# Optimization experiments

Measured on AMD Instinct MI355X. Metric: run time of the kernel, lower is better.

## Reference

```python
import jax, jax.numpy as jnp
import numpy as np

E, G, H = 500000, 256, 256
FRONTIER_BONUS = 0.5
LN_EPS = 1e-5


def setup_inputs() -> dict:
    key = jax.random.key(0)
    ks = jax.random.split(key, 10)
    s = 1.0 / np.sqrt(H)
    edge_tokens = jax.random.normal(ks[0], (E, H), dtype=jnp.float32)
    question_tokens = jax.random.normal(ks[1], (G, H), dtype=jnp.float32)
    edge_batch = jnp.sort(jax.random.randint(ks[2], (E,), 0, G))
    selected_mask = jax.random.randint(ks[3], (E,), 0, 2) == 1
    W_edge = (jax.random.normal(ks[4], (H, H)) * s).astype(jnp.float32)
    W_query = (jax.random.normal(ks[5], (H, H)) * s).astype(jnp.float32)
    att_vec = (jax.random.normal(ks[6], (H,)) * s).astype(jnp.float32)
    ln_g = jnp.ones((2 * H,), jnp.float32)
    ln_b = jnp.zeros((2 * H,), jnp.float32)
    W1 = (jax.random.normal(ks[7], (H, 2 * H)) * (1.0 / np.sqrt(2 * H))).astype(jnp.float32)
    b1 = jnp.zeros((H,), jnp.float32)
    W2 = (jax.random.normal(ks[8], (1, H)) * s).astype(jnp.float32)
    b2 = jnp.zeros((1,), jnp.float32)
    return dict(edge_tokens=edge_tokens, question_tokens=question_tokens,
                edge_batch=edge_batch, selected_mask=selected_mask,
                W_edge=W_edge, W_query=W_query, att_vec=att_vec,
                ln_g=ln_g, ln_b=ln_b, W1=W1, b1=b1, W2=W2, b2=b2)


def reference(edge_tokens, question_tokens, edge_batch, selected_mask,
              W_edge, W_query, att_vec, ln_g, ln_b, W1, b1, W2, b2):
    eps = jnp.finfo(jnp.float32).eps
    candidate_mask = ~selected_mask                      # [E]
    frontier_mask = candidate_mask                       # no current_tail path

    edge_h = edge_tokens @ W_edge.T                      # [E, H]
    q_h = question_tokens @ W_query.T                    # [G, H]

    att_inp = edge_h + q_h[edge_batch]                   # [E, H]
    att_raw = att_inp @ att_vec                          # [E]
    att_raw = jnp.where(att_raw > 0, att_raw, 0.2 * att_raw)  # LeakyReLU(0.2)
    att_raw = att_raw + FRONTIER_BONUS * frontier_mask.astype(jnp.float32)

    # segment softmax over candidate edges of each graph
    max_per_graph = jax.ops.segment_max(att_raw, edge_batch, num_segments=G)
    norm_logits = att_raw - max_per_graph[edge_batch]
    exp = jnp.exp(norm_logits) * candidate_mask.astype(jnp.float32)
    sum_per_graph = jax.ops.segment_sum(exp, edge_batch, num_segments=G)
    edge_probs = exp / jnp.maximum(sum_per_graph, eps)[edge_batch]
    # dropout in eval mode -> identity
    edge_logits = jnp.log(jnp.maximum(edge_probs, eps))  # [E]

    # mean pooling of edge_h per graph
    denom = jnp.maximum(jnp.bincount(edge_batch, length=G), 1).astype(jnp.float32)  # [G]
    pooled_edges = jax.ops.segment_sum(edge_h, edge_batch, num_segments=G) / denom[:, None]

    # stop head: LayerNorm(2H) -> Linear -> GELU -> Linear(1)
    stop_input = jnp.concatenate([pooled_edges, question_tokens], axis=-1)  # [G, 2H]
    mu = stop_input.mean(-1, keepdims=True)
    var = ((stop_input - mu) ** 2).mean(-1, keepdims=True)
    xn = (stop_input - mu) * jax.lax.rsqrt(var + LN_EPS) * ln_g + ln_b
    h1 = jax.nn.gelu(xn @ W1.T + b1, approximate=False)
    stop_logits = (h1 @ W2.T + b2).squeeze(-1)           # [G]

    return edge_logits, stop_logits, pooled_edges
```

## Files before the change

### kernel.cpp

```cpp
#include <hip/hip_runtime.h>
#include <math.h>

#define H   256
#define H2  512
#define FRONTIER_BONUS 0.5f
#define LN_EPS   1e-5f
#define F32_EPS  1.1920929e-07f

__device__ __forceinline__ float block_sum_256(float v, float* sbuf) {
    int tid = threadIdx.x;
    sbuf[tid] = v; __syncthreads();
    for (int s = 128; s > 0; s >>= 1) {
        if (tid < s) sbuf[tid] += sbuf[tid + s];
        __syncthreads();
    }
    float r = sbuf[0]; __syncthreads();
    return r;
}

__device__ __forceinline__ float block_max_256(float v, float* sbuf) {
    int tid = threadIdx.x;
    sbuf[tid] = v; __syncthreads();
    for (int s = 128; s > 0; s >>= 1) {
        if (tid < s) sbuf[tid] = fmaxf(sbuf[tid], sbuf[tid + s]);
        __syncthreads();
    }
    float r = sbuf[0]; __syncthreads();
    return r;
}

__device__ __forceinline__ float wave_sum(float p) {
    #pragma unroll
    for (int off = 1; off < 64; off <<= 1) p += __shfl_xor(p, off, 64);
    return p;
}

__global__ __launch_bounds__(H) void k_uw(const float* __restrict__ W_edge,
                                          const float* __restrict__ W_query,
                                          const float* __restrict__ att_vec,
                                          float* __restrict__ u,
                                          float* __restrict__ w) {
    const float* W = (blockIdx.x == 0) ? W_edge : W_query;
    float* dst     = (blockIdx.x == 0) ? u : w;
    int j = threadIdx.x;
    float acc = 0.f;
    #pragma unroll 8
    for (int i = 0; i < H; ++i) acc += att_vec[i] * W[i * H + j];
    dst[j] = acc;
}

__global__ __launch_bounds__(H) void k_qatt(const float* __restrict__ q,
                                            const float* __restrict__ w,
                                            float* __restrict__ qatt,
                                            float* __restrict__ pooled_sum) {
    __shared__ float sbuf[256];
    int g = blockIdx.x, tid = threadIdx.x;
    pooled_sum[(size_t)g * H + tid] = 0.f;
    float v = q[(size_t)g * H + tid] * w[tid];
    float s = block_sum_256(v, sbuf);
    if (tid == 0) qatt[g] = s;
}

__global__ __launch_bounds__(256) void k_main(const float* __restrict__ edge_tokens,
                                              const int*   __restrict__ edge_batch,
                                              const int*   __restrict__ selected,
                                              const float* __restrict__ u,
                                              const float* __restrict__ qatt,
                                              float* __restrict__ att_raw,
                                              float* __restrict__ pooled_sum,
                                              int E, int chunk) {
    int wave = (blockIdx.x * blockDim.x + threadIdx.x) >> 6;
    int lane = threadIdx.x & 63;
    int e0 = wave * chunk;
    if (e0 >= E) return;
    int e1 = e0 + chunk; if (e1 > E) e1 = E;

    const float4 u4 = ((const float4*)u)[lane];
    const float4* et = (const float4*)edge_tokens;
    float4 acc = make_float4(0.f, 0.f, 0.f, 0.f);
    int cur = edge_batch[e0];

    int e = e0;
    while (e < e1) {
        int n = e1 - e; if (n > 64) n = 64;
        int idx = e + ((lane < n) ? lane : (n - 1));
        int gb  = edge_batch[idx];
        int sel = selected[idx];
        int g0  = __shfl(gb, 0, 64);
        unsigned long long diff = __ballot(gb != g0);
        int run = n;
        if (diff) { int f = (int)__ffsll(diff) - 1; if (f < run) run = f; }

        if (g0 != cur) {
            float* dst = pooled_sum + (size_t)cur * H + lane * 4;
            atomicAdd(dst + 0, acc.x); atomicAdd(dst + 1, acc.y);
            atomicAdd(dst + 2, acc.z); atomicAdd(dst + 3, acc.w);
            acc = make_float4(0.f, 0.f, 0.f, 0.f);
            cur = g0;
        }
        float qa = qatt[g0];
        float my_att = 0.f;

        #pragma unroll 4
        for (int i = 0; i < run; ++i) {
            float4 t = et[(size_t)(e + i) * 64 + lane];
            acc.x += t.x; acc.y += t.y; acc.z += t.z; acc.w += t.w;
            float p = fmaf(t.x, u4.x, fmaf(t.y, u4.y, fmaf(t.z, u4.z, t.w * u4.w)));
            p = wave_sum(p);
            if (i == lane) my_att = p;
        }

        if (lane < run) {
            float a = my_att + qa;
            a = (a > 0.f) ? a : 0.2f * a;
            if (sel == 0) a += FRONTIER_BONUS;
            att_raw[e + lane] = a;
        }
        e += run;
    }
    float* dst = pooled_sum + (size_t)cur * H + lane * 4;
    atomicAdd(dst + 0, acc.x); atomicAdd(dst + 1, acc.y);
    atomicAdd(dst + 2, acc.z); atomicAdd(dst + 3, acc.w);
}

__global__ __launch_bounds__(256) void k_seg(const int*   __restrict__ edge_batch,
                                             const int*   __restrict__ selected,
                                             const float* __restrict__ att_raw,
                                             float* __restrict__ edge_logits,
                                             int*   __restrict__ gcount,
                                             int E) {
    __shared__ float sbuf[256];
    __shared__ int srange[2];
    int g = blockIdx.x, tid = threadIdx.x;
    if (tid == 0) {
        int lo = 0, hi = E;
        while (lo < hi) { int m = (lo + hi) >> 1; if (edge_batch[m] < g) lo = m + 1; else hi = m; }
        srange[0] = lo;
        hi = E;
        while (lo < hi) { int m = (lo + hi) >> 1; if (edge_batch[m] < g + 1) lo = m + 1; else hi = m; }
        srange[1] = lo;
    }
    __syncthreads();
    int s = srange[0], t = srange[1];

    float m = -INFINITY;
    for (int e = s + tid; e < t; e += 256) m = fmaxf(m, att_raw[e]);
    m = block_max_256(m, sbuf);

    float ss = 0.f;
    for (int e = s + tid; e < t; e += 256)
        if (selected[e] == 0) ss += expf(att_raw[e] - m);
    ss = block_sum_256(ss, sbuf);
    float denom = fmaxf(ss, F32_EPS);

    for (int e = s + tid; e < t; e += 256) {
        float ex = (selected[e] == 0) ? expf(att_raw[e] - m) : 0.f;
        float p  = ex / denom;
        edge_logits[e] = logf(fmaxf(p, F32_EPS));
    }
    if (tid == 0) gcount[g] = t - s;
}

__global__ __launch_bounds__(256) void k_pool(const float* __restrict__ pooled_sum,
                                              const int*   __restrict__ gcount,
                                              const float* __restrict__ q,
                                              const float* __restrict__ W_edge,
                                              const float* __restrict__ ln_g,
                                              const float* __restrict__ ln_b,
                                              const float* __restrict__ W1,
                                              const float* __restrict__ b1,
                                              const float* __restrict__ W2,
                                              const float* __restrict__ b2,
                                              float* __restrict__ pooled_out,
                                              float* __restrict__ stop_out) {
    __shared__ __align__(16) float sS[H];
    __shared__ __align__(16) float sP[H];
    __shared__ __align__(16) float sxn[H2];
    __shared__ __align__(16) float sgk[H];
    __shared__ float sbuf[256];
    int g = blockIdx.x, tid = threadIdx.x;
    int lane = tid & 63, wv = tid >> 6;

    sS[tid] = pooled_sum[(size_t)g * H + tid];
    __syncthreads();
    int   cnt = gcount[g];
    float inv = 1.f / (float)(cnt > 1 ? cnt : 1);

    float4 s4 = ((const float4*)sS)[lane];
    for (int r = 0; r < 64; ++r) {
        int i = wv * 64 + r;
        float4 w4 = ((const float4*)(W_edge + (size_t)i * H))[lane];
        float p = fmaf(w4.x, s4.x, fmaf(w4.y, s4.y, fmaf(w4.z, s4.z, w4.w * s4.w)));
        p = wave_sum(p);
        if (lane == 0) sP[i] = p * inv;
    }
    __syncthreads();
    float P = sP[tid];
    pooled_out[(size_t)g * H + tid] = P;

    float x1 = q[(size_t)g * H + tid];
    float mu  = block_sum_256(P + x1, sbuf) * (1.f / (float)H2);
    float d0 = P - mu, d1 = x1 - mu;
    float var = block_sum_256(d0 * d0 + d1 * d1, sbuf) * (1.f / (float)H2);
    float rstd = rsqrtf(var + LN_EPS);
    sxn[tid]     = d0 * rstd * ln_g[tid]     + ln_b[tid];
    sxn[tid + H] = d1 * rstd * ln_g[tid + H] + ln_b[tid + H];
    __syncthreads();

    float4 xa = ((const float4*)sxn)[lane];
    float4 xb = ((const float4*)sxn)[lane + 64];
    for (int r = 0; r < 64; ++r) {
        int k = wv * 64 + r;
        const float4* w1r = (const float4*)(W1 + (size_t)k * H2);
        float4 a0 = w1r[lane], a1 = w1r[lane + 64];
        float p = fmaf(a0.x, xa.x, fmaf(a0.y, xa.y, fmaf(a0.z, xa.z, a0.w * xa.w)))
                + fmaf(a1.x, xb.x, fmaf(a1.y, xb.y, fmaf(a1.z, xb.z, a1.w * xb.w)));
        p = wave_sum(p);
        if (lane == 0) {
            float a = p + b1[k];
            float ge = 0.5f * a * (1.f + erff(a * 0.70710678118654752f));
            sgk[k] = ge * W2[k];
        }
    }
    __syncthreads();
    float tot = block_sum_256(sgk[tid], sbuf);
    if (tid == 0) stop_out[g] = tot + b2[0];
}

extern "C" void kernel_launch(void* const* d_in, const int* in_sizes, int n_in,
                              void* d_out, int out_size, void* d_ws, size_t ws_size,
                              hipStream_t stream) {
    const float* edge_tokens     = (const float*)d_in[0];
    const float* question_tokens = (const float*)d_in[1];
    const int*   edge_batch      = (const int*)  d_in[2];
    const int*   selected        = (const int*)  d_in[3];
    const float* W_edge          = (const float*)d_in[4];
    const float* W_query         = (const float*)d_in[5];
    const float* att_vec         = (const float*)d_in[6];
    const float* ln_g            = (const float*)d_in[7];
    const float* ln_b            = (const float*)d_in[8];
    const float* W1              = (const float*)d_in[9];
    const float* b1              = (const float*)d_in[10];
    const float* W2              = (const float*)d_in[11];
    const float* b2              = (const float*)d_in[12];

    const int E = in_sizes[2];
    const int G = in_sizes[1] / H;

    float* out         = (float*)d_out;
    float* edge_logits = out;
    float* stop_out    = out + E;
    float* pooled_out  = out + E + G;

    float* ws         = (float*)d_ws;
    float* att_raw    = ws;
    float* pooled_sum = ws + E;
    float* u          = pooled_sum + (size_t)G * H;
    float* w          = u + H;
    float* qatt       = w + H;
    int*   gcount     = (int*)(qatt + G);

    k_uw  <<<2, H, 0, stream>>>(W_edge, W_query, att_vec, u, w);
    k_qatt<<<G, H, 0, stream>>>(question_tokens, w, qatt, pooled_sum);

    const int nblocks = 1024;
    const int waves   = nblocks * (256 / 64);
    const int chunk   = (E + waves - 1) / waves;
    k_main<<<nblocks, 256, 0, stream>>>(edge_tokens, edge_batch, selected,
                                        u, qatt, att_raw, pooled_sum, E, chunk);

    k_seg <<<G, 256, 0, stream>>>(edge_batch, selected, att_raw,
                                  edge_logits, gcount, E);
    k_pool<<<G, 256, 0, stream>>>(pooled_sum, gcount, question_tokens, W_edge,
                                  ln_g, ln_b, W1, b1, W2, b2,
                                  pooled_out, stop_out);
}
```

Before: 820.1 us.

## Fuse prologue and epilogue kernels, use nontemporal loads, double main grid

```diff
diff --git a/kernel.cpp b/kernel.cpp
--- a/kernel.cpp
+++ b/kernel.cpp
@@ -6,6 +6,8 @@
 #define FRONTIER_BONUS 0.5f
 #define LN_EPS   1e-5f
 #define F32_EPS  1.1920929e-07f
+
+typedef float v4f __attribute__((ext_vector_type(4)));
 
 __device__ __forceinline__ float block_sum_256(float v, float* sbuf) {
     int tid = threadIdx.x;
@@ -35,28 +37,28 @@
     return p;
 }
 
-__global__ __launch_bounds__(H) void k_uw(const float* __restrict__ W_edge,
-                                          const float* __restrict__ W_query,
-                                          const float* __restrict__ att_vec,
-                                          float* __restrict__ u,
-                                          float* __restrict__ w) {
-    const float* W = (blockIdx.x == 0) ? W_edge : W_query;
-    float* dst     = (blockIdx.x == 0) ? u : w;
-    int j = threadIdx.x;
-    float acc = 0.f;
-    #pragma unroll 8
-    for (int i = 0; i < H; ++i) acc += att_vec[i] * W[i * H + j];
-    dst[j] = acc;
-}
-
-__global__ __launch_bounds__(H) void k_qatt(const float* __restrict__ q,
-                                            const float* __restrict__ w,
-                                            float* __restrict__ qatt,
-                                            float* __restrict__ pooled_sum) {
+__global__ __launch_bounds__(256) void k_pro(const float* __restrict__ W_edge,
+                                             const float* __restrict__ W_query,
+                                             const float* __restrict__ att_vec,
+                                             const float* __restrict__ q,
+                                             float* __restrict__ u,
+                                             float* __restrict__ qatt,
+                                             float* __restrict__ pooled_sum,
+                                             int G) {
     __shared__ float sbuf[256];
     int g = blockIdx.x, tid = threadIdx.x;
+    if (g == G) {
+        float acc = 0.f;
+        #pragma unroll 8
+        for (int i = 0; i < H; ++i) acc += att_vec[i] * W_edge[i * H + tid];
+        u[tid] = acc;
+        return;
+    }
     pooled_sum[(size_t)g * H + tid] = 0.f;
-    float v = q[(size_t)g * H + tid] * w[tid];
+    float wv = 0.f;
+    #pragma unroll 8
+    for (int i = 0; i < H; ++i) wv += att_vec[i] * W_query[i * H + tid];
+    float v = q[(size_t)g * H + tid] * wv;
     float s = block_sum_256(v, sbuf);
     if (tid == 0) qatt[g] = s;
 }
@@ -75,9 +77,9 @@
     if (e0 >= E) return;
     int e1 = e0 + chunk; if (e1 > E) e1 = E;
 
-    const float4 u4 = ((const float4*)u)[lane];
-    const float4* et = (const float4*)edge_tokens;
-    float4 acc = make_float4(0.f, 0.f, 0.f, 0.f);
+    const v4f u4 = ((const v4f*)u)[lane];
+    const v4f* et = (const v4f*)edge_tokens;
+    v4f acc = (v4f)(0.f);
     int cur = edge_batch[e0];
 
     int e = e0;
@@ -95,7 +97,7 @@
             float* dst = pooled_sum + (size_t)cur * H + lane * 4;
             atomicAdd(dst + 0, acc.x); atomicAdd(dst + 1, acc.y);
             atomicAdd(dst + 2, acc.z); atomicAdd(dst + 3, acc.w);
-            acc = make_float4(0.f, 0.f, 0.f, 0.f);
+            acc = (v4f)(0.f);
             cur = g0;
         }
         float qa = qatt[g0];
@@ -103,8 +105,8 @@
 
         #pragma unroll 4
         for (int i = 0; i < run; ++i) {
-            float4 t = et[(size_t)(e + i) * 64 + lane];
-            acc.x += t.x; acc.y += t.y; acc.z += t.z; acc.w += t.w;
+            v4f t = __builtin_nontemporal_load(&et[(size_t)(e + i) * 64 + lane]);
+            acc += t;
             float p = fmaf(t.x, u4.x, fmaf(t.y, u4.y, fmaf(t.z, u4.z, t.w * u4.w)));
             p = wave_sum(p);
             if (i == lane) my_att = p;
@@ -123,56 +125,23 @@
     atomicAdd(dst + 2, acc.z); atomicAdd(dst + 3, acc.w);
 }
 
-__global__ __launch_bounds__(256) void k_seg(const int*   __restrict__ edge_batch,
+__global__ __launch_bounds__(256) void k_epi(const int*   __restrict__ edge_batch,
                                              const int*   __restrict__ selected,
                                              const float* __restrict__ att_raw,
+                                             const float* __restrict__ pooled_sum,
+                                             const float* __restrict__ q,
+                                             const float* __restrict__ W_edge,
+                                             const float* __restrict__ ln_g,
+                                             const float* __restrict__ ln_b,
+                                             const float* __restrict__ W1,
+                                             const float* __restrict__ b1,
+                                             const float* __restrict__ W2,
+                                             const float* __restrict__ b2,
                                              float* __restrict__ edge_logits,
-                                             int*   __restrict__ gcount,
+                                             float* __restrict__ pooled_out,
+                                             float* __restrict__ stop_out,
                                              int E) {
-    __shared__ float sbuf[256];
     __shared__ int srange[2];
-    int g = blockIdx.x, tid = threadIdx.x;
-    if (tid == 0) {
-        int lo = 0, hi = E;
-        while (lo < hi) { int m = (lo + hi) >> 1; if (edge_batch[m] < g) lo = m + 1; else hi = m; }
-        srange[0] = lo;
-        hi = E;
-        while (lo < hi) { int m = (lo + hi) >> 1; if (edge_batch[m] < g + 1) lo = m + 1; else hi = m; }
-        srange[1] = lo;
-    }
-    __syncthreads();
-    int s = srange[0], t = srange[1];
-
-    float m = -INFINITY;
-    for (int e = s + tid; e < t; e += 256) m = fmaxf(m, att_raw[e]);
-    m = block_max_256(m, sbuf);
-
-    float ss = 0.f;
-    for (int e = s + tid; e < t; e += 256)
-        if (selected[e] == 0) ss += expf(att_raw[e] - m);
-    ss = block_sum_256(ss, sbuf);
-    float denom = fmaxf(ss, F32_EPS);
-
-    for (int e = s + tid; e < t; e += 256) {
-        float ex = (selected[e] == 0) ? expf(att_raw[e] - m) : 0.f;
-        float p  = ex / denom;
-        edge_logits[e] = logf(fmaxf(p, F32_EPS));
-    }
-    if (tid == 0) gcount[g] = t - s;
-}
-
-__global__ __launch_bounds__(256) void k_pool(const float* __restrict__ pooled_sum,
-                                              const int*   __restrict__ gcount,
-                                              const float* __restrict__ q,
-                                              const float* __restrict__ W_edge,
-                                              const float* __restrict__ ln_g,
-                                              const float* __restrict__ ln_b,
-                                              const float* __restrict__ W1,
-                                              const float* __restrict__ b1,
-                                              const float* __restrict__ W2,
-                                              const float* __restrict__ b2,
-                                              float* __restrict__ pooled_out,
-                                              float* __restrict__ stop_out) {
     __shared__ __align__(16) float sS[H];
     __shared__ __align__(16) float sP[H];
     __shared__ __align__(16) float sxn[H2];
@@ -181,15 +150,37 @@
     int g = blockIdx.x, tid = threadIdx.x;
     int lane = tid & 63, wv = tid >> 6;
 
+    if (tid < 2) {
+        int target = g + tid, lo = 0, hi = E;
+        while (lo < hi) { int m = (lo + hi) >> 1;
+                          if (edge_batch[m] < target) lo = m + 1; else hi = m; }
+        srange[tid] = lo;
+    }
     sS[tid] = pooled_sum[(size_t)g * H + tid];
     __syncthreads();
-    int   cnt = gcount[g];
+    int s = srange[0], t = srange[1];
+
+    float m = -INFINITY;
+    for (int e = s + tid; e < t; e += 256) m = fmaxf(m, att_raw[e]);
+    m = block_max_256(m, sbuf);
+
+    float ss = 0.f;
+    for (int e = s + tid; e < t; e += 256)
+        if (selected[e] == 0) ss += expf(att_raw[e] - m);
+    ss = block_sum_256(ss, sbuf);
+    float denom = fmaxf(ss, F32_EPS);
+
+    for (int e = s + tid; e < t; e += 256) {
+        float ex = (selected[e] == 0) ? expf(att_raw[e] - m) : 0.f;
+        edge_logits[e] = logf(fmaxf(ex / denom, F32_EPS));
+    }
+
+    int   cnt = t - s;
     float inv = 1.f / (float)(cnt > 1 ? cnt : 1);
-
-    float4 s4 = ((const float4*)sS)[lane];
+    v4f s4 = ((const v4f*)sS)[lane];
     for (int r = 0; r < 64; ++r) {
         int i = wv * 64 + r;
-        float4 w4 = ((const float4*)(W_edge + (size_t)i * H))[lane];
+        v4f w4 = ((const v4f*)(W_edge + (size_t)i * H))[lane];
         float p = fmaf(w4.x, s4.x, fmaf(w4.y, s4.y, fmaf(w4.z, s4.z, w4.w * s4.w)));
         p = wave_sum(p);
         if (lane == 0) sP[i] = p * inv;
@@ -207,12 +198,12 @@
     sxn[tid + H] = d1 * rstd * ln_g[tid + H] + ln_b[tid + H];
     __syncthreads();
 
-    float4 xa = ((const float4*)sxn)[lane];
-    float4 xb = ((const float4*)sxn)[lane + 64];
+    v4f xa = ((const v4f*)sxn)[lane];
+    v4f xb = ((const v4f*)sxn)[lane + 64];
     for (int r = 0; r < 64; ++r) {
         int k = wv * 64 + r;
-        const float4* w1r = (const float4*)(W1 + (size_t)k * H2);
-        float4 a0 = w1r[lane], a1 = w1r[lane + 64];
+        const v4f* w1r = (const v4f*)(W1 + (size_t)k * H2);
+        v4f a0 = w1r[lane], a1 = w1r[lane + 64];
         float p = fmaf(a0.x, xa.x, fmaf(a0.y, xa.y, fmaf(a0.z, xa.z, a0.w * xa.w)))
                 + fmaf(a1.x, xb.x, fmaf(a1.y, xb.y, fmaf(a1.z, xb.z, a1.w * xb.w)));
         p = wave_sum(p);
@@ -256,22 +247,19 @@
     float* att_raw    = ws;
     float* pooled_sum = ws + E;
     float* u          = pooled_sum + (size_t)G * H;
-    float* w          = u + H;
-    float* qatt       = w + H;
-    int*   gcount     = (int*)(qatt + G);
-
-    k_uw  <<<2, H, 0, stream>>>(W_edge, W_query, att_vec, u, w);
-    k_qatt<<<G, H, 0, stream>>>(question_tokens, w, qatt, pooled_sum);
-
-    const int nblocks = 1024;
+    float* qatt       = u + H;
+
+    k_pro<<<G + 1, 256, 0, stream>>>(W_edge, W_query, att_vec, question_tokens,
+                                     u, qatt, pooled_sum, G);
+
+    const int nblocks = 2048;
     const int waves   = nblocks * (256 / 64);
     const int chunk   = (E + waves - 1) / waves;
     k_main<<<nblocks, 256, 0, stream>>>(edge_tokens, edge_batch, selected,
                                         u, qatt, att_raw, pooled_sum, E, chunk);
 
-    k_seg <<<G, 256, 0, stream>>>(edge_batch, selected, att_raw,
-                                  edge_logits, gcount, E);
-    k_pool<<<G, 256, 0, stream>>>(pooled_sum, gcount, question_tokens, W_edge,
-                                  ln_g, ln_b, W1, b1, W2, b2,
-                                  pooled_out, stop_out);
-}
+    k_epi<<<G, 256, 0, stream>>>(edge_batch, selected, att_raw, pooled_sum,
+                                 question_tokens, W_edge, ln_g, ln_b,
+                                 W1, b1, W2, b2,
+                                 edge_logits, pooled_out, stop_out, E);
+}
```

Result: faster. 766.0 us (-6.6%).
